# Kernel tuning notes

Hardware: AMD Instinct MI355X
Metric: run time of the kernel (lower is better)

## Reference

```python
import jax, jax.numpy as jnp
import numpy as np

HID = 128      # hidden_dim
CDIM = 128     # c_dim
NBLK = 5       # n_blocks
RESO = 32      # grid_resolution
G = RESO ** 3  # number of voxels
B, T = 2, 100000


def setup_inputs() -> dict:
    key = jax.random.key(0)
    ks = jax.random.split(key, 8)
    return {
        "points": jax.random.normal(ks[0], (B, T, 3), jnp.float32),
        "index": jax.random.randint(ks[1], (B, 1, T), 0, G, dtype=jnp.int64),
        # fc_pos: Linear(3, 2*HID)
        "fc_pos_w": jax.random.normal(ks[2], (3, 2 * HID), jnp.float32) * 0.1,
        "fc_pos_b": jnp.zeros((2 * HID,), jnp.float32),
        # ResnetBlockFC(2*HID, HID) x NBLK: fc_0 (2H->H), fc_1 (H->H), shortcut (2H->H, no bias)
        "fc0_w": jax.random.normal(ks[3], (NBLK, 2 * HID, HID), jnp.float32) * 0.05,
        "fc0_b": jnp.zeros((NBLK, HID), jnp.float32),
        "fc1_w": jax.random.normal(ks[4], (NBLK, HID, HID), jnp.float32) * 0.05,
        "fc1_b": jnp.zeros((NBLK, HID), jnp.float32),
        "sc_w": jax.random.normal(ks[5], (NBLK, 2 * HID, HID), jnp.float32) * 0.05,
        # fc_c: Linear(HID, CDIM)
        "fc_c_w": jax.random.normal(ks[6], (HID, CDIM), jnp.float32) * 0.05,
        "fc_c_b": jnp.zeros((CDIM,), jnp.float32),
    }


def _resnet_block(x, w0, b0, w1, b1, ws):
    # ResnetBlockFC: net = fc_0(relu(x)); dx = fc_1(relu(net)); out = shortcut(x) + dx
    net = jnp.maximum(x, 0.0) @ w0 + b0
    dx = jnp.maximum(net, 0.0) @ w1 + b1
    return x @ ws + dx


def reference(points, index, fc_pos_w, fc_pos_b, fc0_w, fc0_b, fc1_w, fc1_b, sc_w, fc_c_w, fc_c_b):
    idx = index[:, 0, :]  # [B, T]

    def pool_local(net):
        # scatter_max over voxels, then gather back per point
        seg = jax.vmap(lambda c_b, i_b: jax.ops.segment_max(c_b, i_b, num_segments=G))(net, idx)  # [B,G,H]
        return jnp.take_along_axis(seg, idx[:, :, None], axis=1)  # [B,T,H]; every gathered voxel is non-empty

    net = points @ fc_pos_w + fc_pos_b          # [B,T,2H]
    net = _resnet_block(net, fc0_w[0], fc0_b[0], fc1_w[0], fc1_b[0], sc_w[0])  # [B,T,H]
    for i in range(1, NBLK):
        pooled = pool_local(net)
        net = jnp.concatenate([net, pooled], axis=2)  # [B,T,2H]
        net = _resnet_block(net, fc0_w[i], fc0_b[i], fc1_w[i], fc1_b[i], sc_w[i])

    c = net @ fc_c_w + fc_c_b  # [B,T,CDIM]

    # generate_grid_features: scatter_mean into the 32^3 grid (zeros for empty voxels)
    sums = jax.vmap(lambda c_b, i_b: jax.ops.segment_sum(c_b, i_b, num_segments=G))(c, idx)  # [B,G,CDIM]
    cnts = jax.vmap(lambda i_b: jax.ops.segment_sum(jnp.ones((T,), c.dtype), i_b, num_segments=G))(idx)  # [B,G]
    cnts = cnts[:, :, None]
    mean = jnp.where(cnts > 0, sums / jnp.maximum(cnts, 1.0), 0.0)
    fea_grid = jnp.transpose(mean, (0, 2, 1)).reshape(B, CDIM, RESO, RESO, RESO)
    return fea_grid
```

## Files before the change

kernel.cpp:

```cpp
#include <hip/hip_runtime.h>

#define T_PTS 100000
#define NB 2
#define GCELLS 32768
#define NCELL (NB * GCELLS)
#define HID 128
#define MBLK 64
#define RBPB 1563
#define GRID_RB (NB * RBPB)

typedef __attribute__((ext_vector_type(8))) short bf16x8;
typedef __attribute__((ext_vector_type(4))) float f32x4;

#define MFMA16 __builtin_amdgcn_mfma_f32_16x16x32_bf16

__device__ __forceinline__ unsigned short bf16rne(float f) {
  unsigned u = __float_as_uint(f);
  return (unsigned short)((u + 0x7FFFu + ((u >> 16) & 1u)) >> 16);
}
__device__ __forceinline__ unsigned packhl(float f) {
  unsigned short h = bf16rne(f);
  float hf = __uint_as_float(((unsigned)h) << 16);
  unsigned short l = bf16rne(f - hf);
  return (((unsigned)h) << 16) | (unsigned)l;
}

union U8 { bf16x8 v; unsigned u[4]; };

__device__ __forceinline__ void up2(unsigned w0, unsigned w1, unsigned& h,
                                    unsigned& l) {
  h = __builtin_amdgcn_perm(w1, w0, 0x07060302u);
  l = __builtin_amdgcn_perm(w1, w0, 0x05040100u);
}

__device__ __forceinline__ void dma16(const unsigned* g, unsigned* l) {
  __builtin_amdgcn_global_load_lds(
      (const __attribute__((address_space(1))) unsigned*)g,
      (__attribute__((address_space(3))) unsigned*)l, 16, 0, 0);
}

template <int MODE>
__global__ __launch_bounds__(256, 4) void resblock_mfma(
    const void* __restrict__ srcv, const float* __restrict__ posw,
    const float* __restrict__ posb, const unsigned* __restrict__ cell,
    const int* __restrict__ idx, const unsigned short* __restrict__ w0p,
    const float* __restrict__ b0, const unsigned short* __restrict__ w1p,
    const float* __restrict__ b1, const unsigned short* __restrict__ swp,
    unsigned* __restrict__ net_out) {
  __shared__ unsigned lds32[8192];
  const int tid = threadIdx.x;
  const int lane = tid & 63;
  const int wid = tid >> 6;
  const int wc = wid;
  const int b = blockIdx.x / RBPB;
  const int t0 = (blockIdx.x % RBPB) * MBLK;
  const int valid = (T_PTS - t0 < MBLK) ? (T_PTS - t0) : MBLK;

  const int srow = wid * 16 + (lane & 15);
  const int skc = (lane >> 4) * 8;
  const int ptc = (t0 + srow < T_PTS) ? srow : (T_PTS - 1 - t0);
  const unsigned* nrowL = nullptr;
  const unsigned* crowL = nullptr;
  float pp0 = 0.f, pp1 = 0.f, pp2 = 0.f;
  if (MODE == 1) {
    const long prow = (long)b * T_PTS + t0 + ptc;
    nrowL = (const unsigned*)srcv + prow * HID;
    crowL = cell + ((long)b * GCELLS + idx[prow]) * HID;
  } else {
    const float* ppp = (const float*)srcv + ((long)b * T_PTS + t0 + ptc) * 3;
    pp0 = ppp[0]; pp1 = ppp[1]; pp2 = ppp[2];
  }

  auto stage = [&](int ks) {
    unsigned* base = &lds32[(ks & 1) * 2048 + wid * 512];
    if (MODE == 1) {
      const unsigned* rp =
          ((ks < 4) ? nrowL + ks * 32 : crowL + (ks - 4) * 32) + skc;
      dma16(rp, base);
      dma16(rp + 4, base + 256);
    } else {
      const int kb = ks * 32 + skc;
      float xv[8];
#pragma unroll
      for (int i = 0; i < 8; i += 4) {
        float4 wa = *(const float4*)(posw + kb + i);
        float4 wb = *(const float4*)(posw + 256 + kb + i);
        float4 wcc = *(const float4*)(posw + 512 + kb + i);
        float4 bb = *(const float4*)(posb + kb + i);
        xv[i + 0] = fmaf(pp0, wa.x, fmaf(pp1, wb.x, fmaf(pp2, wcc.x, bb.x)));
        xv[i + 1] = fmaf(pp0, wa.y, fmaf(pp1, wb.y, fmaf(pp2, wcc.y, bb.y)));
        xv[i + 2] = fmaf(pp0, wa.z, fmaf(pp1, wb.z, fmaf(pp2, wcc.z, bb.z)));
        xv[i + 3] = fmaf(pp0, wa.w, fmaf(pp1, wb.w, fmaf(pp2, wcc.w, bb.w)));
      }
      unsigned w[8];
#pragma unroll
      for (int i = 0; i < 8; ++i) w[i] = packhl(xv[i]);
      unsigned* p = base + lane * 4;
      uint4 q;
      q.x = w[0]; q.y = w[1]; q.z = w[2]; q.w = w[3];
      *(uint4*)p = q;
      q.x = w[4]; q.y = w[5]; q.z = w[6]; q.w = w[7];
      *(uint4*)(p + 256) = q;
    }
  };

  auto load_B = [&](const unsigned short* base, int loOff, int ks, bf16x8* h,
                    bf16x8* l) {
#pragma unroll
    for (int nt = 0; nt < 2; ++nt) {
      const int fi = (ks * 8 + wc * 2 + nt) * 512 + lane * 8;
      h[nt] = *(const bf16x8*)(base + fi);
      l[nt] = *(const bf16x8*)(base + loOff + fi);
    }
  };

  f32x4 accy[4][2], acco[4][2];
#pragma unroll
  for (int i = 0; i < 4; ++i)
#pragma unroll
    for (int j = 0; j < 2; ++j) {
      f32x4 z = {0.f, 0.f, 0.f, 0.f};
      accy[i][j] = z;
      acco[i][j] = z;
    }

  stage(0);
  __syncthreads();

#pragma unroll 1
  for (int ks = 0; ks < 8; ++ks) {
    const int sb = (ks & 1) << 11;
    bf16x8 bh[2], bl[2];
    load_B(w0p, 32768, ks, bh, bl);
    if (ks < 7) stage(ks + 1);
    __builtin_amdgcn_s_setprio(1);
#pragma unroll
    for (int mt = 0; mt < 4; ++mt) {
      const unsigned* p = &lds32[sb + mt * 512 + lane * 4];
      uint4 q1 = *(const uint4*)p;
      uint4 q2 = *(const uint4*)(p + 256);
      unsigned q[8] = {q1.x, q1.y, q1.z, q1.w, q2.x, q2.y, q2.z, q2.w};
      U8 rh, rl;
#pragma unroll
      for (int p2 = 0; p2 < 4; ++p2) {
        const unsigned w0 = q[2 * p2], w1 = q[2 * p2 + 1];
        const unsigned r0 = ((int)w0 < 0) ? 0u : w0;
        const unsigned r1 = ((int)w1 < 0) ? 0u : w1;
        up2(r0, r1, rh.u[p2], rl.u[p2]);
      }
#pragma unroll
      for (int nt = 0; nt < 2; ++nt) {
        accy[mt][nt] = MFMA16(rh.v, bh[nt], accy[mt][nt], 0, 0, 0);
        accy[mt][nt] = MFMA16(rh.v, bl[nt], accy[mt][nt], 0, 0, 0);
        accy[mt][nt] = MFMA16(rl.v, bh[nt], accy[mt][nt], 0, 0, 0);
      }
    }
    __builtin_amdgcn_s_setprio(0);
    asm volatile("" ::: "memory");
    load_B(swp, 32768, ks, bh, bl);
    __builtin_amdgcn_s_setprio(1);
#pragma unroll
    for (int mt = 0; mt < 4; ++mt) {
      const unsigned* p = &lds32[sb + mt * 512 + lane * 4];
      uint4 q1 = *(const uint4*)p;
      uint4 q2 = *(const uint4*)(p + 256);
      unsigned q[8] = {q1.x, q1.y, q1.z, q1.w, q2.x, q2.y, q2.z, q2.w};
      U8 xh, xl;
#pragma unroll
      for (int p2 = 0; p2 < 4; ++p2)
        up2(q[2 * p2], q[2 * p2 + 1], xh.u[p2], xl.u[p2]);
#pragma unroll
      for (int nt = 0; nt < 2; ++nt) {
        acco[mt][nt] = MFMA16(xh.v, bh[nt], acco[mt][nt], 0, 0, 0);
        acco[mt][nt] = MFMA16(xh.v, bl[nt], acco[mt][nt], 0, 0, 0);
        acco[mt][nt] = MFMA16(xl.v, bh[nt], acco[mt][nt], 0, 0, 0);
      }
    }
    __builtin_amdgcn_s_setprio(0);
    __syncthreads();
  }

  {
    float b0v[2];
#pragma unroll
    for (int nt = 0; nt < 2; ++nt)
      b0v[nt] = b0[wc * 32 + nt * 16 + (lane & 15)];
#pragma unroll
    for (int mt = 0; mt < 4; ++mt) {
#pragma unroll
      for (int nt = 0; nt < 2; ++nt) {
        const int c = wc * 32 + nt * 16 + (lane & 15);
        const int k2 = c >> 5;
        const int j = c & 7;
        const int lahi = ((c & 31) >> 3) * 16;
#pragma unroll
        for (int r = 0; r < 4; ++r) {
          float h = fmaxf(accy[mt][nt][r] + b0v[nt], 0.f);
          int la = lahi + (lane >> 4) * 4 + r;
          la ^= (la >> 3) & 7;
          lds32[((k2 * 4 + mt) * 64 + la) * 8 + j] = packhl(h);
        }
      }
    }
  }
  __syncthreads();

  {
    const int lar2 = lane ^ ((lane >> 3) & 7);
#pragma unroll
    for (int k2 = 0; k2 < 4; ++k2) {
      bf16x8 ch[2], cl[2];
      load_B(w1p, 16384, k2, ch, cl);
      __builtin_amdgcn_s_setprio(1);
#pragma unroll
      for (int mt = 0; mt < 4; ++mt) {
        const unsigned* p = &lds32[((k2 * 4 + mt) * 64 + lar2) * 8];
        uint4 q1 = *(const uint4*)p;
        uint4 q2 = *(const uint4*)(p + 4);
        unsigned q[8] = {q1.x, q1.y, q1.z, q1.w, q2.x, q2.y, q2.z, q2.w};
        U8 ah, al;
#pragma unroll
        for (int p2 = 0; p2 < 4; ++p2)
          up2(q[2 * p2], q[2 * p2 + 1], ah.u[p2], al.u[p2]);
#pragma unroll
        for (int nt = 0; nt < 2; ++nt) {
          acco[mt][nt] = MFMA16(ah.v, ch[nt], acco[mt][nt], 0, 0, 0);
          acco[mt][nt] = MFMA16(ah.v, cl[nt], acco[mt][nt], 0, 0, 0);
          acco[mt][nt] = MFMA16(al.v, ch[nt], acco[mt][nt], 0, 0, 0);
        }
      }
      __builtin_amdgcn_s_setprio(0);
    }
  }

  {
    float b1v[2];
#pragma unroll
    for (int nt = 0; nt < 2; ++nt)
      b1v[nt] = b1[wc * 32 + nt * 16 + (lane & 15)];
#pragma unroll
    for (int mt = 0; mt < 4; ++mt) {
#pragma unroll
      for (int r = 0; r < 4; ++r) {
        const int row = mt * 16 + (lane >> 4) * 4 + r;
        if (row < valid) {
          unsigned* op = net_out + ((long)b * T_PTS + t0 + row) * HID;
          op[wc * 32 + (lane & 15)] = packhl(acco[mt][0][r] + b1v[0]);
          op[wc * 32 + 16 + (lane & 15)] = packhl(acco[mt][1][r] + b1v[1]);
        }
      }
    }
  }
}

__global__ __launch_bounds__(256, 4) void final_mfma(
    unsigned* __restrict__ net, const unsigned short* __restrict__ wcp,
    const float* __restrict__ bc) {
  __shared__ unsigned lds32[4096];
  const int tid = threadIdx.x;
  const int lane = tid & 63;
  const int wid = tid >> 6;
  const int wc = wid;
  const int b = blockIdx.x / RBPB;
  const int t0 = (blockIdx.x % RBPB) * MBLK;
  const int valid = (T_PTS - t0 < MBLK) ? (T_PTS - t0) : MBLK;

  const int srow = wid * 16 + (lane & 15);
  const int skc = (lane >> 4) * 8;
  const int ptc = (t0 + srow < T_PTS) ? srow : (T_PTS - 1 - t0);
  const unsigned* nrowL = net + ((long)b * T_PTS + t0 + ptc) * HID;

  auto stage = [&](int ks) {
    unsigned* base = &lds32[(ks & 1) * 2048 + wid * 512];
    const unsigned* rp = nrowL + ks * 32 + skc;
    dma16(rp, base);
    dma16(rp + 4, base + 256);
  };
  auto load_B = [&](int ks, bf16x8* h, bf16x8* l) {
#pragma unroll
    for (int nt = 0; nt < 2; ++nt) {
      const int fi = (ks * 8 + wc * 2 + nt) * 512 + lane * 8;
      h[nt] = *(const bf16x8*)(wcp + fi);
      l[nt] = *(const bf16x8*)(wcp + 16384 + fi);
    }
  };

  f32x4 acc[4][2];
#pragma unroll
  for (int i = 0; i < 4; ++i)
#pragma unroll
    for (int j = 0; j < 2; ++j) {
      f32x4 z = {0.f, 0.f, 0.f, 0.f};
      acc[i][j] = z;
    }

  stage(0);
  __syncthreads();

#pragma unroll 1
  for (int ks = 0; ks < 4; ++ks) {
    const int sb = (ks & 1) << 11;
    bf16x8 ch[2], cl[2];
    load_B(ks, ch, cl);
    if (ks < 3) stage(ks + 1);
    __builtin_amdgcn_s_setprio(1);
#pragma unroll
    for (int mt = 0; mt < 4; ++mt) {
      const unsigned* p = &lds32[sb + mt * 512 + lane * 4];
      uint4 q1 = *(const uint4*)p;
      uint4 q2 = *(const uint4*)(p + 256);
      unsigned q[8] = {q1.x, q1.y, q1.z, q1.w, q2.x, q2.y, q2.z, q2.w};
      U8 ah, al;
#pragma unroll
      for (int p2 = 0; p2 < 4; ++p2)
        up2(q[2 * p2], q[2 * p2 + 1], ah.u[p2], al.u[p2]);
#pragma unroll
      for (int nt = 0; nt < 2; ++nt) {
        acc[mt][nt] = MFMA16(ah.v, ch[nt], acc[mt][nt], 0, 0, 0);
        acc[mt][nt] = MFMA16(ah.v, cl[nt], acc[mt][nt], 0, 0, 0);
        acc[mt][nt] = MFMA16(al.v, ch[nt], acc[mt][nt], 0, 0, 0);
      }
    }
    __builtin_amdgcn_s_setprio(0);
    __syncthreads();
  }

  float* fout = (float*)net;
  float bcv[2];
#pragma unroll
  for (int nt = 0; nt < 2; ++nt)
    bcv[nt] = bc[wc * 32 + nt * 16 + (lane & 15)];
#pragma unroll
  for (int mt = 0; mt < 4; ++mt) {
#pragma unroll
    for (int r = 0; r < 4; ++r) {
      const int row = mt * 16 + (lane >> 4) * 4 + r;
      if (row < valid) {
        float* op = fout + ((long)b * T_PTS + t0 + row) * HID;
        op[wc * 32 + (lane & 15)] = acc[mt][0][r] + bcv[0];
        op[wc * 32 + 16 + (lane & 15)] = acc[mt][1][r] + bcv[1];
      }
    }
  }
}

__global__ void pack_weights(const float* __restrict__ fc0,
                             const float* __restrict__ fc1,
                             const float* __restrict__ sc,
                             const float* __restrict__ fcc,
                             unsigned short* __restrict__ w0p,
                             unsigned short* __restrict__ w1p,
                             unsigned short* __restrict__ swp,
                             unsigned short* __restrict__ wcp) {
  int gid = blockIdx.x * 256 + threadIdx.x;
  const float* src;
  unsigned short* dst;
  int K, e;
  if (gid < 163840) { src = fc0; dst = w0p; K = 256; e = gid; }
  else if (gid < 327680) { src = sc; dst = swp; K = 256; e = gid - 163840; }
  else if (gid < 409600) { src = fc1; dst = w1p; K = 128; e = gid - 327680; }
  else if (gid < 425984) { src = fcc; dst = wcp; K = 128; e = gid - 409600; }
  else return;
  const int mat = e / (K * 128);
  const int r = e - mat * K * 128;
  const int k = r >> 7, n = r & 127;
  const float x = src[e];
  const unsigned short hi = bf16rne(x);
  const float hf = __uint_as_float(((unsigned)hi) << 16);
  const unsigned short lo = bf16rne(x - hf);
  const int ks = k >> 5, lg = (k >> 3) & 3, j = k & 7;
  const int l = lg * 16 + (n & 15), nt = n >> 4;
  unsigned short* mb = dst + (long)mat * K * 256;
  const int off = ((ks * 8 + nt) * 64 + l) * 8 + j;
  mb[off] = hi;
  mb[off + K * 128] = lo;
}

__global__ void zero_i32(int* __restrict__ p, int n) {
  const int i = blockIdx.x * 256 + threadIdx.x;
  if (i < n) p[i] = 0;
}

__global__ void count_csr(const int* __restrict__ idx, int* __restrict__ curs) {
  const int gid = blockIdx.x * 256 + threadIdx.x;
  if (gid >= NB * T_PTS) return;
  const int b = gid / T_PTS;
  atomicAdd(&curs[b * GCELLS + idx[gid]], 1);
}

__global__ __launch_bounds__(1024) void scan_csr(const int* __restrict__ cnt,
                                                 int* __restrict__ offsets) {
  __shared__ int part[1024];
  const int t = threadIdx.x;
  const int base = t * (NCELL / 1024);
  int s = 0;
  for (int i = 0; i < NCELL / 1024; ++i) s += cnt[base + i];
  part[t] = s;
  __syncthreads();
  for (int d = 1; d < 1024; d <<= 1) {
    int v = (t >= d) ? part[t - d] : 0;
    __syncthreads();
    part[t] += v;
    __syncthreads();
  }
  int run = (t == 0) ? 0 : part[t - 1];
  for (int i = 0; i < NCELL / 1024; ++i) {
    offsets[base + i] = run;
    run += cnt[base + i];
  }
  if (t == 1023) offsets[NCELL] = run;
}

__global__ void scatter_csr(const int* __restrict__ idx,
                            const int* __restrict__ offsets,
                            int* __restrict__ curs, int* __restrict__ perm) {
  const int gid = blockIdx.x * 256 + threadIdx.x;
  if (gid >= NB * T_PTS) return;
  const int b = gid / T_PTS;
  const int cellk = b * GCELLS + idx[gid];
  const int slot = offsets[cellk] + atomicAdd(&curs[cellk], 1);
  perm[slot] = gid;
}

__global__ __launch_bounds__(256) void pool_csr(const unsigned* __restrict__ net,
                                                const int* __restrict__ perm,
                                                const int* __restrict__ offsets,
                                                unsigned* __restrict__ cellf) {
  const int cellk = blockIdx.x * 4 + (threadIdx.x >> 6);
  const int lane = threadIdx.x & 63;
  const int s0 = offsets[cellk], s1 = offsets[cellk + 1];
  if (s0 >= s1) return;
  float m0 = -3.402823466e38f, m1 = -3.402823466e38f;
  unsigned b0 = 0u, b1 = 0u;
  for (int j = s0; j < s1; ++j) {
    const long row = perm[j];
    uint2 w = *(const uint2*)(net + row * HID + lane * 2);
    float v0 = __uint_as_float(w.x & 0xFFFF0000u) + __uint_as_float(w.x << 16);
    float v1 = __uint_as_float(w.y & 0xFFFF0000u) + __uint_as_float(w.y << 16);
    if (v0 > m0) { m0 = v0; b0 = w.x; }
    if (v1 > m1) { m1 = v1; b1 = w.y; }
  }
  uint2 o; o.x = b0; o.y = b1;
  *(uint2*)(cellf + (long)cellk * HID + lane * 2) = o;
}

__global__ __launch_bounds__(256) void cellsum_csr(
    const float* __restrict__ c, const int* __restrict__ perm,
    const int* __restrict__ offsets, float* __restrict__ sums) {
  const int cellk = blockIdx.x * 4 + (threadIdx.x >> 6);
  const int lane = threadIdx.x & 63;
  const int s0 = offsets[cellk], s1 = offsets[cellk + 1];
  if (s0 >= s1) return;
  float2 m = {0.f, 0.f};
  for (int j = s0; j < s1; ++j) {
    const long row = perm[j];
    float2 v = *(const float2*)(c + row * HID + lane * 2);
    m.x += v.x;
    m.y += v.y;
  }
  *(float2*)(sums + (long)cellk * HID + lane * 2) = m;
}

__global__ void mean_kernel(const float* __restrict__ sums,
                            const int* __restrict__ offsets,
                            float* __restrict__ out) {
  const long gid = (long)blockIdx.x * 256 + threadIdx.x;
  if (gid >= (long)NB * HID * GCELLS) return;
  const int g = (int)(gid % GCELLS);
  const int c = (int)((gid / GCELLS) % HID);
  const int b = (int)(gid / ((long)HID * GCELLS));
  const int cellk = b * GCELLS + g;
  const int cnt = offsets[cellk + 1] - offsets[cellk];
  out[gid] = cnt > 0 ? sums[(long)cellk * HID + c] / (float)cnt : 0.f;
}

extern "C" void kernel_launch(void* const* d_in, const int* in_sizes, int n_in,
                              void* d_out, int out_size, void* d_ws,
                              size_t ws_size, hipStream_t stream) {
  const float* points = (const float*)d_in[0];
  const int* idx = (const int*)d_in[1];
  const float* fc_pos_w = (const float*)d_in[2];
  const float* fc_pos_b = (const float*)d_in[3];
  const float* fc0_w = (const float*)d_in[4];
  const float* fc0_b = (const float*)d_in[5];
  const float* fc1_w = (const float*)d_in[6];
  const float* fc1_b = (const float*)d_in[7];
  const float* sc_w = (const float*)d_in[8];
  const float* fc_c_w = (const float*)d_in[9];
  const float* fc_c_b = (const float*)d_in[10];
  float* out = (float*)d_out;

  const long NET_BYTES = (long)NB * T_PTS * HID * 4;
  const long CELL_BYTES = (long)NB * GCELLS * HID * 4;
  unsigned* net = (unsigned*)d_ws;
  unsigned* cellf = (unsigned*)((char*)d_ws + NET_BYTES);
  float* sums = (float*)cellf;
  int* offsets = (int*)((char*)d_ws + NET_BYTES + CELL_BYTES);

  unsigned short* packs = (unsigned short*)d_out;
  unsigned short* w0p = packs;
  unsigned short* swp = packs + 327680;
  unsigned short* w1p = packs + 655360;
  unsigned short* wcp = packs + 819200;
  int* curs = (int*)((char*)d_out + (2l << 20));
  int* perm = (int*)((char*)d_out + (3l << 20));

  const int GRID_PTS = (NB * T_PTS + 255) / 256;
  const int GRID_ZERO = (NCELL + 255) / 256;
  const int GRID_CELL = NCELL / 4;
  const int GRID_MEAN = NB * HID * GCELLS / 256;

  pack_weights<<<1664, 256, 0, stream>>>(fc0_w, fc1_w, sc_w, fc_c_w, w0p, w1p,
                                         swp, wcp);

  zero_i32<<<GRID_ZERO, 256, 0, stream>>>(curs, NCELL);
  count_csr<<<GRID_PTS, 256, 0, stream>>>(idx, curs);
  scan_csr<<<1, 1024, 0, stream>>>(curs, offsets);
  zero_i32<<<GRID_ZERO, 256, 0, stream>>>(curs, NCELL);
  scatter_csr<<<GRID_PTS, 256, 0, stream>>>(idx, offsets, curs, perm);

  resblock_mfma<0><<<GRID_RB, 256, 0, stream>>>(
      points, fc_pos_w, fc_pos_b, nullptr, nullptr, w0p, fc0_b, w1p, fc1_b,
      swp, net);

  for (int i = 1; i < 5; ++i) {
    pool_csr<<<GRID_CELL, 256, 0, stream>>>(net, perm, offsets, cellf);
    resblock_mfma<1><<<GRID_RB, 256, 0, stream>>>(
        net, nullptr, nullptr, cellf, idx, w0p + (long)i * 65536,
        fc0_b + i * HID, w1p + (long)i * 32768, fc1_b + i * HID,
        swp + (long)i * 65536, net);
  }

  final_mfma<<<GRID_RB, 256, 0, stream>>>(net, wcp, fc_c_b);
  cellsum_csr<<<GRID_CELL, 256, 0, stream>>>((const float*)net, perm, offsets,
                                             sums);
  mean_kernel<<<GRID_MEAN, 256, 0, stream>>>(sums, offsets, out);
}
```

Before: 801.3 us.

## Store activations as split hi/lo bf16 planes and precompute ReLU operands in LDS

Changes the per-row activation layout from interleaved hi/lo packed words to separate hi-plane and lo-plane halves. MFMA A-operands can then be read straight from LDS without per-tile byte permutes. For the first matmul, the ReLU'd hi/lo operands are derived once per k-step into extra LDS buffers instead of being recomputed per MFMA tile. The LDS double-buffer layout, staging order and the pool kernel are adapted to match, at the cost of more LDS traffic, an explicit vmcnt wait, and narrower 16-bit global stores in the epilogue.

```diff
diff --git a/kernel.cpp b/kernel.cpp
--- a/kernel.cpp
+++ b/kernel.cpp
@@ -18,10 +18,14 @@
   unsigned u = __float_as_uint(f);
   return (unsigned short)((u + 0x7FFFu + ((u >> 16) & 1u)) >> 16);
 }
+__device__ __forceinline__ void bf16split(float f, unsigned short& h,
+                                          unsigned short& l) {
+  h = bf16rne(f);
+  l = bf16rne(f - __uint_as_float(((unsigned)h) << 16));
+}
 __device__ __forceinline__ unsigned packhl(float f) {
-  unsigned short h = bf16rne(f);
-  float hf = __uint_as_float(((unsigned)h) << 16);
-  unsigned short l = bf16rne(f - hf);
+  unsigned short h, l;
+  bf16split(f, h, l);
   return (((unsigned)h) << 16) | (unsigned)l;
 }
 
@@ -31,6 +35,13 @@
                                     unsigned& l) {
   h = __builtin_amdgcn_perm(w1, w0, 0x07060302u);
   l = __builtin_amdgcn_perm(w1, w0, 0x05040100u);
+}
+
+__device__ __forceinline__ void relu2(unsigned qh, unsigned ql, unsigned& rh,
+                                      unsigned& rl) {
+  const unsigned keep = ((~qh >> 15) & 0x00010001u) * 0xFFFFu;
+  rh = qh & keep;
+  rl = ql & keep;
 }
 
 __device__ __forceinline__ void dma16(const unsigned* g, unsigned* l) {
@@ -57,7 +68,7 @@
   const int valid = (T_PTS - t0 < MBLK) ? (T_PTS - t0) : MBLK;
 
   const int srow = wid * 16 + (lane & 15);
-  const int skc = (lane >> 4) * 8;
+  const int skc4 = (lane >> 4) * 4;
   const int ptc = (t0 + srow < T_PTS) ? srow : (T_PTS - 1 - t0);
   const unsigned* nrowL = nullptr;
   const unsigned* crowL = nullptr;
@@ -71,39 +82,57 @@
     pp0 = ppp[0]; pp1 = ppp[1]; pp2 = ppp[2];
   }
 
-  auto stage = [&](int ks) {
-    unsigned* base = &lds32[(ks & 1) * 2048 + wid * 512];
-    if (MODE == 1) {
-      const unsigned* rp =
-          ((ks < 4) ? nrowL + ks * 32 : crowL + (ks - 4) * 32) + skc;
-      dma16(rp, base);
-      dma16(rp + 4, base + 256);
-    } else {
-      const int kb = ks * 32 + skc;
-      float xv[8];
-#pragma unroll
-      for (int i = 0; i < 8; i += 4) {
-        float4 wa = *(const float4*)(posw + kb + i);
-        float4 wb = *(const float4*)(posw + 256 + kb + i);
-        float4 wcc = *(const float4*)(posw + 512 + kb + i);
-        float4 bb = *(const float4*)(posb + kb + i);
-        xv[i + 0] = fmaf(pp0, wa.x, fmaf(pp1, wb.x, fmaf(pp2, wcc.x, bb.x)));
-        xv[i + 1] = fmaf(pp0, wa.y, fmaf(pp1, wb.y, fmaf(pp2, wcc.y, bb.y)));
-        xv[i + 2] = fmaf(pp0, wa.z, fmaf(pp1, wb.z, fmaf(pp2, wcc.z, bb.z)));
-        xv[i + 3] = fmaf(pp0, wa.w, fmaf(pp1, wb.w, fmaf(pp2, wcc.w, bb.w)));
-      }
-      unsigned w[8];
-#pragma unroll
-      for (int i = 0; i < 8; ++i) w[i] = packhl(xv[i]);
-      unsigned* p = base + lane * 4;
-      uint4 q;
-      q.x = w[0]; q.y = w[1]; q.z = w[2]; q.w = w[3];
-      *(uint4*)p = q;
-      q.x = w[4]; q.y = w[5]; q.z = w[6]; q.w = w[7];
-      *(uint4*)(p + 256) = q;
-    }
+  auto stage_dma = [&](int ks) {
+    unsigned* base = &lds32[((ks & 1) << 12) + wid * 256];
+    const unsigned* rowp = (ks < 4) ? nrowL : crowL;
+    const int ko = ((ks & 3) << 4) + skc4;
+    dma16(rowp + ko, base);
+    dma16(rowp + 64 + ko, base + 1024);
   };
-
+  auto derive = [&](int ks) {
+    const int db = ((ks & 1) << 12) + wid * 256 + lane * 4;
+    uint4 qh = *(const uint4*)&lds32[db];
+    uint4 ql = *(const uint4*)&lds32[db + 1024];
+    uint4 rh, rl;
+    relu2(qh.x, ql.x, rh.x, rl.x);
+    relu2(qh.y, ql.y, rh.y, rl.y);
+    relu2(qh.z, ql.z, rh.z, rl.z);
+    relu2(qh.w, ql.w, rh.w, rl.w);
+    *(uint4*)&lds32[db + 2048] = rh;
+    *(uint4*)&lds32[db + 3072] = rl;
+  };
+  auto stage0 = [&](int ks) {
+    const int kb = ks * 32 + (lane >> 4) * 8;
+    float xv[8];
+#pragma unroll
+    for (int i = 0; i < 8; i += 4) {
+      float4 wa = *(const float4*)(posw + kb + i);
+      float4 wb = *(const float4*)(posw + 256 + kb + i);
+      float4 wcc = *(const float4*)(posw + 512 + kb + i);
+      float4 bb = *(const float4*)(posb + kb + i);
+      xv[i + 0] = fmaf(pp0, wa.x, fmaf(pp1, wb.x, fmaf(pp2, wcc.x, bb.x)));
+      xv[i + 1] = fmaf(pp0, wa.y, fmaf(pp1, wb.y, fmaf(pp2, wcc.y, bb.y)));
+      xv[i + 2] = fmaf(pp0, wa.z, fmaf(pp1, wb.z, fmaf(pp2, wcc.z, bb.z)));
+      xv[i + 3] = fmaf(pp0, wa.w, fmaf(pp1, wb.w, fmaf(pp2, wcc.w, bb.w)));
+    }
+    unsigned ph[8];
+#pragma unroll
+    for (int i = 0; i < 8; ++i) ph[i] = packhl(xv[i]);
+    uint4 xh4, xl4, rh4, rl4;
+    up2(ph[0], ph[1], xh4.x, xl4.x);
+    up2(ph[2], ph[3], xh4.y, xl4.y);
+    up2(ph[4], ph[5], xh4.z, xl4.z);
+    up2(ph[6], ph[7], xh4.w, xl4.w);
+    relu2(xh4.x, xl4.x, rh4.x, rl4.x);
+    relu2(xh4.y, xl4.y, rh4.y, rl4.y);
+    relu2(xh4.z, xl4.z, rh4.z, rl4.z);
+    relu2(xh4.w, xl4.w, rh4.w, rl4.w);
+    const int db = ((ks & 1) << 12) + wid * 256 + lane * 4;
+    *(uint4*)&lds32[db] = xh4;
+    *(uint4*)&lds32[db + 1024] = xl4;
+    *(uint4*)&lds32[db + 2048] = rh4;
+    *(uint4*)&lds32[db + 3072] = rl4;
+  };
   auto load_B = [&](const unsigned short* base, int loOff, int ks, bf16x8* h,
                     bf16x8* l) {
 #pragma unroll
@@ -124,59 +153,58 @@
       acco[i][j] = z;
     }
 
-  stage(0);
+  if (MODE == 1) {
+    stage_dma(0);
+    asm volatile("s_waitcnt vmcnt(0)" ::: "memory");
+    derive(0);
+  } else {
+    stage0(0);
+  }
   __syncthreads();
 
 #pragma unroll 1
   for (int ks = 0; ks < 8; ++ks) {
-    const int sb = (ks & 1) << 11;
+    const int sb = (ks & 1) << 12;
     bf16x8 bh[2], bl[2];
     load_B(w0p, 32768, ks, bh, bl);
-    if (ks < 7) stage(ks + 1);
     __builtin_amdgcn_s_setprio(1);
 #pragma unroll
     for (int mt = 0; mt < 4; ++mt) {
-      const unsigned* p = &lds32[sb + mt * 512 + lane * 4];
-      uint4 q1 = *(const uint4*)p;
-      uint4 q2 = *(const uint4*)(p + 256);
-      unsigned q[8] = {q1.x, q1.y, q1.z, q1.w, q2.x, q2.y, q2.z, q2.w};
-      U8 rh, rl;
-#pragma unroll
-      for (int p2 = 0; p2 < 4; ++p2) {
-        const unsigned w0 = q[2 * p2], w1 = q[2 * p2 + 1];
-        const unsigned r0 = ((int)w0 < 0) ? 0u : w0;
-        const unsigned r1 = ((int)w1 < 0) ? 0u : w1;
-        up2(r0, r1, rh.u[p2], rl.u[p2]);
-      }
+      const unsigned* pr = &lds32[sb + 2048 + mt * 256 + lane * 4];
+      bf16x8 rh = *(const bf16x8*)pr;
+      bf16x8 rl = *(const bf16x8*)(pr + 1024);
 #pragma unroll
       for (int nt = 0; nt < 2; ++nt) {
-        accy[mt][nt] = MFMA16(rh.v, bh[nt], accy[mt][nt], 0, 0, 0);
-        accy[mt][nt] = MFMA16(rh.v, bl[nt], accy[mt][nt], 0, 0, 0);
-        accy[mt][nt] = MFMA16(rl.v, bh[nt], accy[mt][nt], 0, 0, 0);
+        accy[mt][nt] = MFMA16(rh, bh[nt], accy[mt][nt], 0, 0, 0);
+        accy[mt][nt] = MFMA16(rh, bl[nt], accy[mt][nt], 0, 0, 0);
+        accy[mt][nt] = MFMA16(rl, bh[nt], accy[mt][nt], 0, 0, 0);
       }
     }
     __builtin_amdgcn_s_setprio(0);
-    asm volatile("" ::: "memory");
     load_B(swp, 32768, ks, bh, bl);
+    if (MODE == 1 && ks < 7) stage_dma(ks + 1);
     __builtin_amdgcn_s_setprio(1);
 #pragma unroll
     for (int mt = 0; mt < 4; ++mt) {
-      const unsigned* p = &lds32[sb + mt * 512 + lane * 4];
-      uint4 q1 = *(const uint4*)p;
-      uint4 q2 = *(const uint4*)(p + 256);
-      unsigned q[8] = {q1.x, q1.y, q1.z, q1.w, q2.x, q2.y, q2.z, q2.w};
-      U8 xh, xl;
-#pragma unroll
-      for (int p2 = 0; p2 < 4; ++p2)
-        up2(q[2 * p2], q[2 * p2 + 1], xh.u[p2], xl.u[p2]);
+      const unsigned* px = &lds32[sb + mt * 256 + lane * 4];
+      bf16x8 xh = *(const bf16x8*)px;
+      bf16x8 xl = *(const bf16x8*)(px + 1024);
 #pragma unroll
       for (int nt = 0; nt < 2; ++nt) {
-        acco[mt][nt] = MFMA16(xh.v, bh[nt], acco[mt][nt], 0, 0, 0);
-        acco[mt][nt] = MFMA16(xh.v, bl[nt], acco[mt][nt], 0, 0, 0);
-        acco[mt][nt] = MFMA16(xl.v, bh[nt], acco[mt][nt], 0, 0, 0);
+        acco[mt][nt] = MFMA16(xh, bh[nt], acco[mt][nt], 0, 0, 0);
+        acco[mt][nt] = MFMA16(xh, bl[nt], acco[mt][nt], 0, 0, 0);
+        acco[mt][nt] = MFMA16(xl, bh[nt], acco[mt][nt], 0, 0, 0);
       }
     }
     __builtin_amdgcn_s_setprio(0);
+    if (ks < 7) {
+      if (MODE == 1) {
+        asm volatile("s_waitcnt vmcnt(0)" ::: "memory");
+        derive(ks + 1);
+      } else {
+        stage0(ks + 1);
+      }
+    }
     __syncthreads();
   }
 
@@ -244,9 +272,15 @@
       for (int r = 0; r < 4; ++r) {
         const int row = mt * 16 + (lane >> 4) * 4 + r;
         if (row < valid) {
-          unsigned* op = net_out + ((long)b * T_PTS + t0 + row) * HID;
-          op[wc * 32 + (lane & 15)] = packhl(acco[mt][0][r] + b1v[0]);
-          op[wc * 32 + 16 + (lane & 15)] = packhl(acco[mt][1][r] + b1v[1]);
+          unsigned short* op =
+              (unsigned short*)(net_out + ((long)b * T_PTS + t0 + row) * HID);
+          unsigned short h, l;
+          bf16split(acco[mt][0][r] + b1v[0], h, l);
+          op[wc * 32 + (lane & 15)] = h;
+          op[128 + wc * 32 + (lane & 15)] = l;
+          bf16split(acco[mt][1][r] + b1v[1], h, l);
+          op[wc * 32 + 16 + (lane & 15)] = h;
+          op[128 + wc * 32 + 16 + (lane & 15)] = l;
         }
       }
     }
@@ -266,15 +300,15 @@
   const int valid = (T_PTS - t0 < MBLK) ? (T_PTS - t0) : MBLK;
 
   const int srow = wid * 16 + (lane & 15);
-  const int skc = (lane >> 4) * 8;
+  const int skc4 = (lane >> 4) * 4;
   const int ptc = (t0 + srow < T_PTS) ? srow : (T_PTS - 1 - t0);
   const unsigned* nrowL = net + ((long)b * T_PTS + t0 + ptc) * HID;
 
   auto stage = [&](int ks) {
-    unsigned* base = &lds32[(ks & 1) * 2048 + wid * 512];
-    const unsigned* rp = nrowL + ks * 32 + skc;
-    dma16(rp, base);
-    dma16(rp + 4, base + 256);
+    unsigned* base = &lds32[((ks & 1) << 11) + wid * 256];
+    const int ko = (ks << 4) + skc4;
+    dma16(nrowL + ko, base);
+    dma16(nrowL + 64 + ko, base + 1024);
   };
   auto load_B = [&](int ks, bf16x8* h, bf16x8* l) {
 #pragma unroll
@@ -306,19 +340,14 @@
     __builtin_amdgcn_s_setprio(1);
 #pragma unroll
     for (int mt = 0; mt < 4; ++mt) {
-      const unsigned* p = &lds32[sb + mt * 512 + lane * 4];
-      uint4 q1 = *(const uint4*)p;
-      uint4 q2 = *(const uint4*)(p + 256);
-      unsigned q[8] = {q1.x, q1.y, q1.z, q1.w, q2.x, q2.y, q2.z, q2.w};
-      U8 ah, al;
-#pragma unroll
-      for (int p2 = 0; p2 < 4; ++p2)
-        up2(q[2 * p2], q[2 * p2 + 1], ah.u[p2], al.u[p2]);
+      const unsigned* px = &lds32[sb + mt * 256 + lane * 4];
+      bf16x8 xh = *(const bf16x8*)px;
+      bf16x8 xl = *(const bf16x8*)(px + 1024);
 #pragma unroll
       for (int nt = 0; nt < 2; ++nt) {
-        acc[mt][nt] = MFMA16(ah.v, ch[nt], acc[mt][nt], 0, 0, 0);
-        acc[mt][nt] = MFMA16(ah.v, cl[nt], acc[mt][nt], 0, 0, 0);
-        acc[mt][nt] = MFMA16(al.v, ch[nt], acc[mt][nt], 0, 0, 0);
+        acc[mt][nt] = MFMA16(xh, ch[nt], acc[mt][nt], 0, 0, 0);
+        acc[mt][nt] = MFMA16(xh, cl[nt], acc[mt][nt], 0, 0, 0);
+        acc[mt][nt] = MFMA16(xl, ch[nt], acc[mt][nt], 0, 0, 0);
       }
     }
     __builtin_amdgcn_s_setprio(0);
@@ -365,9 +394,8 @@
   const int r = e - mat * K * 128;
   const int k = r >> 7, n = r & 127;
   const float x = src[e];
-  const unsigned short hi = bf16rne(x);
-  const float hf = __uint_as_float(((unsigned)hi) << 16);
-  const unsigned short lo = bf16rne(x - hf);
+  unsigned short hi, lo;
+  bf16split(x, hi, lo);
   const int ks = k >> 5, lg = (k >> 3) & 3, j = k & 7;
   const int l = lg * 16 + (n & 15), nt = n >> 4;
   unsigned short* mb = dst + (long)mat * K * 256;
@@ -431,17 +459,21 @@
   const int s0 = offsets[cellk], s1 = offsets[cellk + 1];
   if (s0 >= s1) return;
   float m0 = -3.402823466e38f, m1 = -3.402823466e38f;
-  unsigned b0 = 0u, b1 = 0u;
+  unsigned h0 = 0u, l0 = 0u, h1 = 0u, l1 = 0u;
   for (int j = s0; j < s1; ++j) {
     const long row = perm[j];
-    uint2 w = *(const uint2*)(net + row * HID + lane * 2);
-    float v0 = __uint_as_float(w.x & 0xFFFF0000u) + __uint_as_float(w.x << 16);
-    float v1 = __uint_as_float(w.y & 0xFFFF0000u) + __uint_as_float(w.y << 16);
-    if (v0 > m0) { m0 = v0; b0 = w.x; }
-    if (v1 > m1) { m1 = v1; b1 = w.y; }
-  }
-  uint2 o; o.x = b0; o.y = b1;
-  *(uint2*)(cellf + (long)cellk * HID + lane * 2) = o;
+    const unsigned* rp = net + row * HID;
+    unsigned hi = rp[lane];
+    unsigned lo = rp[64 + lane];
+    float v0 = __uint_as_float(hi << 16) + __uint_as_float(lo << 16);
+    float v1 = __uint_as_float(hi & 0xFFFF0000u) +
+               __uint_as_float(lo & 0xFFFF0000u);
+    if (v0 > m0) { m0 = v0; h0 = hi; l0 = lo; }
+    if (v1 > m1) { m1 = v1; h1 = hi; l1 = lo; }
+  }
+  unsigned* cp = cellf + (long)cellk * HID;
+  cp[lane] = (h0 & 0xFFFFu) | (h1 & 0xFFFF0000u);
+  cp[64 + lane] = (l0 & 0xFFFFu) | (l1 & 0xFFFF0000u);
 }
 
 __global__ __launch_bounds__(256) void cellsum_csr(
```

Result: no change. 794.5 us (-0.8%).
